# Kernel optimization log

Measured on AMD Instinct MI355X. Metric: run time of the kernel, lower is better.

## Reference

```python
import jax, jax.numpy as jnp
import numpy as np

N_NODES = 50000
N_EDGES = 500000
HIDDEN = 128
HEADS = 8
HEAD_DIM = HIDDEN // HEADS


def setup_inputs() -> dict:
    key = jax.random.key(0)
    ks = jax.random.split(key, 20)

    def lin_w(k, fin, fout):
        return (jax.random.normal(k, (fin, fout), jnp.float32) / np.sqrt(fin)).astype(jnp.float32)

    inp = {
        "h": jax.random.normal(ks[0], (N_NODES, HIDDEN), jnp.float32),
        "x": jax.random.normal(ks[1], (N_NODES, 3), jnp.float32),
        "src": jax.random.randint(ks[2], (N_EDGES,), 0, N_NODES, jnp.int32),
        "dst": jax.random.randint(ks[3], (N_EDGES,), 0, N_NODES, jnp.int32),
        "distances": jax.random.uniform(ks[4], (N_EDGES,), jnp.float32),
        # linear layers stored as [in, out] (transposed vs torch nn.Linear)
        "Wq": lin_w(ks[5], HIDDEN, HIDDEN), "bq": jnp.zeros((HIDDEN,), jnp.float32),
        "Wk": lin_w(ks[6], HIDDEN, HIDDEN), "bk": jnp.zeros((HIDDEN,), jnp.float32),
        "Wv": lin_w(ks[7], HIDDEN, HIDDEN), "bv": jnp.zeros((HIDDEN,), jnp.float32),
        "Wo": lin_w(ks[8], HIDDEN, HIDDEN), "bo": jnp.zeros((HIDDEN,), jnp.float32),
        "Wd": lin_w(ks[9], 1, HEADS), "bd": jnp.zeros((HEADS,), jnp.float32),
        "Wg1": lin_w(ks[10], HIDDEN, HIDDEN), "bg1": jnp.zeros((HIDDEN,), jnp.float32),
        "Wg2": lin_w(ks[11], HIDDEN, 1), "bg2": jnp.zeros((1,), jnp.float32),
    }
    return inp


def reference(h, x, src, dst, distances,
              Wq, bq, Wk, bk, Wv, bv, Wo, bo, Wd, bd, Wg1, bg1, Wg2, bg2):
    n = h.shape[0]
    heads = Wd.shape[1]
    dh = Wq.shape[1] // heads

    q = (h @ Wq + bq).reshape(n, heads, dh)
    k = (h @ Wk + bk).reshape(n, heads, dh)
    v = (h @ Wv + bv).reshape(n, heads, dh)

    q_src = q[src]            # [E, heads, dh]
    k_dst = k[dst]
    v_dst = v[dst]

    logits = jnp.einsum('ehd,ehd->eh', q_src, k_dst) / jnp.sqrt(jnp.asarray(dh, h.dtype))
    bias = (distances * distances)[:, None] @ Wd + bd      # [E, heads]
    lg = logits - bias

    # segment softmax over edges grouped by src node
    m = jax.ops.segment_max(lg, src, num_segments=n)        # [N, heads]
    ex = jnp.exp(lg - m[src])
    s = jax.ops.segment_sum(ex, src, num_segments=n)
    w = ex / jnp.maximum(s[src], 1e-9)                      # [E, heads]

    h_upd = jax.ops.segment_sum(v_dst * w[:, :, None], src, num_segments=n)
    h_out = h + h_upd.reshape(n, heads * dh) @ Wo + bo

    w_mean = w.mean(axis=1)                                 # mean over heads -> [E]
    disp = jax.ops.segment_sum((x[dst] - x[src]) * w_mean[:, None], src, num_segments=n)

    gate = jnp.tanh(jax.nn.silu(h_out @ Wg1 + bg1) @ Wg2 + bg2)  # [N, 1]
    x_out = x + gate * disp
    return (h_out, x_out)
```

## Files before the change

### kernel.cpp

```cpp
#include <hip/hip_runtime.h>
#include <math.h>

#define N_NODES 50000
#define N_EDGES 500000
#define HIDDEN 128
#define HEADS 8
#define HEAD_DIM 16

#define QB 391
#define QKV_TOTAL 782
#define SCAT_BLOCKS 1954
#define SPLITW_BLOCKS 320
#define ZERO_BLOCKS 196

typedef __attribute__((ext_vector_type(8))) short short8;
typedef __attribute__((ext_vector_type(4))) float floatx4;

#define OFF_Q       0u
#define OFF_KV      6400000u
#define OFF_HHI     12800000u
#define OFF_HLO     16000000u
#define OFF_DISP    19200000u
#define OFF_CNT     19350016u
#define OFF_ROWPTR  19400032u
#define OFF_CURSOR  19450048u
#define OFF_ESD     19500064u
#define OFF_WSPLIT  20500064u

static __device__ __forceinline__ unsigned short f2bf(float f) {
    unsigned u = __builtin_bit_cast(unsigned, f);
    unsigned r = (u + 0x7FFFu + ((u >> 16) & 1u)) >> 16;
    return (unsigned short)r;
}
static __device__ __forceinline__ float bf2f(unsigned short s) {
    return __builtin_bit_cast(float, (unsigned)s << 16);
}

__global__ void k_prep(const float* __restrict__ Wq, const float* __restrict__ Wk,
                       const float* __restrict__ Wv, const float* __restrict__ Wo,
                       const float* __restrict__ Wg1, unsigned short* __restrict__ ws,
                       int* __restrict__ cnt) {
    if (blockIdx.x >= SPLITW_BLOCKS) {
        int i = (int)(blockIdx.x - SPLITW_BLOCKS) * 256 + threadIdx.x;
        if (i < N_NODES) cnt[i] = 0;
        return;
    }
    int t = blockIdx.x * 256 + threadIdx.x;
    int m = t >> 14, r = t & 16383;
    int k = r >> 7, n = r & 127;
    const float* W = (m == 0) ? Wq : (m == 1) ? Wk : (m == 2) ? Wv : (m == 3) ? Wo : Wg1;
    float x = W[k * 128 + n];
    int kc = k >> 5, kin = k & 31, quad = kin >> 3, j = kin & 7;
    int ct = n >> 4, nin = n & 15, lane = quad * 16 + nin;
    unsigned base = ((((unsigned)(m * 4 + kc) * 8 + ct) * 2) * 64 + lane) * 8 + j;
    unsigned short a = f2bf(x);
    ws[base] = a;
    ws[base + 512] = f2bf(x - bf2f(a));
}

__global__ void k_count(const int* __restrict__ src, int* __restrict__ cnt,
                        int* __restrict__ rnk) {
    int e = blockIdx.x * 256 + threadIdx.x;
    if (e < N_EDGES) rnk[e] = atomicAdd(&cnt[src[e]], 1);
}

__global__ __launch_bounds__(1024) void k_scan1(const int* __restrict__ cnt,
                                                int* __restrict__ loc,
                                                int* __restrict__ bsum, int n) {
    __shared__ int buf[1024];
    int t = threadIdx.x;
    int i = blockIdx.x * 1024 + t;
    int val = (i < n) ? cnt[i] : 0;
    buf[t] = val;
    __syncthreads();
    for (int off = 1; off < 1024; off <<= 1) {
        int a = (t >= off) ? buf[t - off] : 0;
        __syncthreads();
        buf[t] += a;
        __syncthreads();
    }
    if (i < n) loc[i] = buf[t];
    if (t == 1023) bsum[blockIdx.x] = buf[1023];
}

__global__ __launch_bounds__(256) void k_scan23(const int* __restrict__ loc,
                                                const int* __restrict__ bsum,
                                                int* __restrict__ rowptr, int n, int nb) {
    __shared__ int sb[64];
    int t = threadIdx.x;
    if (t < 64) {
        int v = (t < nb) ? bsum[t] : 0;
        for (int off = 1; off < 64; off <<= 1) {
            int a = __shfl_up(v, off);
            if (t >= off) v += a;
        }
        sb[t] = v;
    }
    __syncthreads();
    int i = blockIdx.x * 256 + t;
    if (i < n) {
        int off = (i >= 1024) ? sb[(i >> 10) - 1] : 0;
        rowptr[i + 1] = loc[i] + off;
    }
    if (i == 0) rowptr[0] = 0;
}

__global__ __launch_bounds__(256, 2) void k_qkv_scatter(
    const float* __restrict__ h, const unsigned short* __restrict__ wsp,
    const float* __restrict__ bq, const float* __restrict__ bk, const float* __restrict__ bv,
    float* __restrict__ q, unsigned* __restrict__ kvp,
    const int* __restrict__ src, const int* __restrict__ dst,
    const float* __restrict__ dist, const int* __restrict__ rowptr,
    const int* __restrict__ rnk, int2* __restrict__ esd) {
    if (blockIdx.x >= QKV_TOTAL) {
        int e = (int)(blockIdx.x - QKV_TOTAL) * 256 + threadIdx.x;
        if (e < N_EDGES) {
            int s = src[e];
            float dd = dist[e];
            int pos = rowptr[s] + rnk[e];
            esd[pos] = make_int2(dst[e], __float_as_int(dd * dd));
        }
        return;
    }

    __shared__ short lds[32768];
    const int tid = threadIdx.x;
    const int wave = tid >> 6, lane = tid & 63;
    const int quad = lane >> 4, l15 = lane & 15;
    const bool iskv = (blockIdx.x >= QB);
    const int blk = iskv ? (int)blockIdx.x - QB : (int)blockIdx.x;
    const int row0 = blk * 128 + wave * 32;

    short8 ah[2][4], al[2][4];
#pragma unroll
    for (int rt = 0; rt < 2; ++rt) {
        int row = row0 + rt * 16 + l15;
        if (row >= N_NODES) row = N_NODES - 1;
        const float* hp = h + (size_t)row * 128;
#pragma unroll
        for (int kc = 0; kc < 4; ++kc) {
            const float* p = hp + kc * 32 + quad * 8;
            float4 f0 = *(const float4*)(p);
            float4 f1 = *(const float4*)(p + 4);
            float fv[8] = {f0.x, f0.y, f0.z, f0.w, f1.x, f1.y, f1.z, f1.w};
#pragma unroll
            for (int j = 0; j < 8; ++j) {
                unsigned short hi = f2bf(fv[j]);
                ah[rt][kc][j] = (short)hi;
                al[rt][kc][j] = (short)f2bf(fv[j] - bf2f(hi));
            }
        }
    }

    auto stage = [&](int m) {
        const float4* s4 = (const float4*)(wsp + (unsigned)m * 32768u);
        float4* d4 = (float4*)lds;
#pragma unroll 4
        for (int it = tid; it < 4096; it += 256) d4[it] = s4[it];
    };

    auto compute = [&](floatx4 (&acc)[2][8]) {
#pragma unroll
        for (int kc = 0; kc < 4; ++kc) {
#pragma unroll
            for (int ct = 0; ct < 8; ++ct) {
                const short* tb = lds + (((kc * 8 + ct) * 2) * 64 + lane) * 8;
                short8 bh = *(const short8*)(tb);
                short8 bl = *(const short8*)(tb + 512);
#pragma unroll
                for (int rt = 0; rt < 2; ++rt) {
                    acc[rt][ct] = __builtin_amdgcn_mfma_f32_16x16x32_bf16(
                        ah[rt][kc], bh, acc[rt][ct], 0, 0, 0);
                    acc[rt][ct] = __builtin_amdgcn_mfma_f32_16x16x32_bf16(
                        ah[rt][kc], bl, acc[rt][ct], 0, 0, 0);
                    acc[rt][ct] = __builtin_amdgcn_mfma_f32_16x16x32_bf16(
                        al[rt][kc], bh, acc[rt][ct], 0, 0, 0);
                }
            }
        }
    };

    if (!iskv) {
        stage(0);
        __syncthreads();
        floatx4 acc[2][8];
#pragma unroll
        for (int rt = 0; rt < 2; ++rt)
#pragma unroll
            for (int ct = 0; ct < 8; ++ct) acc[rt][ct] = (floatx4){0.f, 0.f, 0.f, 0.f};
        compute(acc);
#pragma unroll
        for (int ct = 0; ct < 8; ++ct) {
            int col = ct * 16 + l15;
            float b = bq[col];
#pragma unroll
            for (int rt = 0; rt < 2; ++rt)
#pragma unroll
                for (int reg = 0; reg < 4; ++reg) {
                    int row = row0 + rt * 16 + quad * 4 + reg;
                    if (row < N_NODES) q[(size_t)row * 128 + col] = acc[rt][ct][reg] + b;
                }
        }
    } else {
        stage(1);
        __syncthreads();
        floatx4 acc[2][8];
#pragma unroll
        for (int rt = 0; rt < 2; ++rt)
#pragma unroll
            for (int ct = 0; ct < 8; ++ct) acc[rt][ct] = (floatx4){0.f, 0.f, 0.f, 0.f};
        compute(acc);
        unsigned kb[2][8][2];
#pragma unroll
        for (int ct = 0; ct < 8; ++ct) {
            float b = bk[ct * 16 + l15];
#pragma unroll
            for (int rt = 0; rt < 2; ++rt) {
                kb[rt][ct][0] = (unsigned)f2bf(acc[rt][ct][0] + b) |
                                ((unsigned)f2bf(acc[rt][ct][1] + b) << 16);
                kb[rt][ct][1] = (unsigned)f2bf(acc[rt][ct][2] + b) |
                                ((unsigned)f2bf(acc[rt][ct][3] + b) << 16);
            }
        }
        __syncthreads();
        stage(2);
        __syncthreads();
#pragma unroll
        for (int rt = 0; rt < 2; ++rt)
#pragma unroll
            for (int ct = 0; ct < 8; ++ct) acc[rt][ct] = (floatx4){0.f, 0.f, 0.f, 0.f};
        compute(acc);
#pragma unroll
        for (int ct = 0; ct < 8; ++ct) {
            int col = ct * 16 + l15;
            float b = bv[col];
#pragma unroll
            for (int rt = 0; rt < 2; ++rt)
#pragma unroll
                for (int reg = 0; reg < 4; ++reg) {
                    int row = row0 + rt * 16 + quad * 4 + reg;
                    unsigned vb = f2bf(acc[rt][ct][reg] + b);
                    unsigned kw = (kb[rt][ct][reg >> 1] >> ((reg & 1) * 16)) & 0xFFFFu;
                    if (row < N_NODES) kvp[(size_t)row * 128 + col] = kw | (vb << 16);
                }
        }
    }
}

__global__ __launch_bounds__(256) void k_edge_node(
    const float* __restrict__ q, const unsigned* __restrict__ kvp,
    const float* __restrict__ x,
    const int2* __restrict__ esd, const int* __restrict__ rowptr,
    const float* __restrict__ Wd, const float* __restrict__ bd,
    unsigned short* __restrict__ hupd_hi, unsigned short* __restrict__ hupd_lo,
    float* __restrict__ disp) {
    const int wave = threadIdx.x >> 6, lane = threadIdx.x & 63;
    const int node = blockIdx.x * 4 + wave;
    const int h = lane >> 3, sub = lane & 7;
    const int beg = rowptr[node], end = rowptr[node + 1];

    const float2 qv = *(const float2*)(q + (size_t)node * 128 + 2 * lane);
    const float wdh = Wd[h], bdh = bd[h];
    const bool dal = (sub < 3);
    float xs = dal ? x[node * 3 + sub] : 0.f;
    const unsigned colo = 2 * lane;

    float acc0 = 0.f, acc1 = 0.f, s_own = 0.f, da = 0.f;

    for (int cb = beg; cb < end; cb += 64) {
        int idx = cb + lane;
        int dvec = 0; float d2vec = 0.f;
        if (idx < end) {
            int2 ed = esd[idx];
            dvec = ed.x;
            d2vec = __int_as_float(ed.y);
        }
        int clen = min(64, end - cb);
        int i = 0;
        for (; i + 4 <= clen; i += 4) {
            int di[4]; float dd2[4]; uint2 kv2[4]; float xg[4];
#pragma unroll
            for (int j = 0; j < 4; ++j) {
                di[j]  = __shfl(dvec, i + j);
                dd2[j] = __shfl(d2vec, i + j);
            }
#pragma unroll
            for (int j = 0; j < 4; ++j)
                kv2[j] = *(const uint2*)(kvp + (unsigned)di[j] * 128u + colo);
#pragma unroll
            for (int j = 0; j < 4; ++j)
                xg[j] = dal ? x[(unsigned)di[j] * 3u + sub] : 0.f;
#pragma unroll
            for (int j = 0; j < 4; ++j) {
                float k0 = __builtin_bit_cast(float, kv2[j].x << 16);
                float v0 = __builtin_bit_cast(float, kv2[j].x & 0xFFFF0000u);
                float k1 = __builtin_bit_cast(float, kv2[j].y << 16);
                float v1 = __builtin_bit_cast(float, kv2[j].y & 0xFFFF0000u);
                float p = qv.x * k0 + qv.y * k1;
                p += __shfl_xor(p, 1);
                p += __shfl_xor(p, 2);
                p += __shfl_xor(p, 4);
                float w = __expf(p * 0.25f - (dd2[j] * wdh + bdh));
                s_own += w;
                acc0 += v0 * w;
                acc1 += v1 * w;
                da += (xg[j] - xs) * w;
            }
        }
        for (; i < clen; ++i) {
            int dij  = __shfl(dvec, i);
            float d2 = __shfl(d2vec, i);
            uint2 kv2 = *(const uint2*)(kvp + (unsigned)dij * 128u + colo);
            float xgj = dal ? x[(unsigned)dij * 3u + sub] : 0.f;
            float k0 = __builtin_bit_cast(float, kv2.x << 16);
            float v0 = __builtin_bit_cast(float, kv2.x & 0xFFFF0000u);
            float k1 = __builtin_bit_cast(float, kv2.y << 16);
            float v1 = __builtin_bit_cast(float, kv2.y & 0xFFFF0000u);
            float p = qv.x * k0 + qv.y * k1;
            p += __shfl_xor(p, 1);
            p += __shfl_xor(p, 2);
            p += __shfl_xor(p, 4);
            float w = __expf(p * 0.25f - (d2 * wdh + bdh));
            s_own += w;
            acc0 += v0 * w;
            acc1 += v1 * w;
            da += (xgj - xs) * w;
        }
    }

    float inva = 1.f / fmaxf(s_own, 1e-9f);
    float o0 = acc0 * inva, o1 = acc1 * inva;
    unsigned short h0 = f2bf(o0), h1 = f2bf(o1);
    unsigned short l0 = f2bf(o0 - bf2f(h0)), l1 = f2bf(o1 - bf2f(h1));
    ((unsigned*)hupd_hi)[(size_t)node * 64 + lane] = (unsigned)h0 | ((unsigned)h1 << 16);
    ((unsigned*)hupd_lo)[(size_t)node * 64 + lane] = (unsigned)l0 | ((unsigned)l1 << 16);

    da *= 0.125f * inva;
    da += __shfl_xor(da, 8);
    da += __shfl_xor(da, 16);
    da += __shfl_xor(da, 32);
    if (lane < 3) disp[node * 3 + lane] = da;
}

__global__ __launch_bounds__(256) void k_hout_gate(
    const float* __restrict__ h,
    const unsigned short* __restrict__ hupd_hi, const unsigned short* __restrict__ hupd_lo,
    const unsigned short* __restrict__ wsp,
    const float* __restrict__ bo, const float* __restrict__ bg1,
    const float* __restrict__ Wg2, const float* __restrict__ bg2,
    const float* __restrict__ x, const float* __restrict__ disp,
    float* __restrict__ hout, float* __restrict__ xout) {
    __shared__ float hb[4][16 * 132];
    const int wave = threadIdx.x >> 6, lane = threadIdx.x & 63;
    const int quad = lane >> 4, l15 = lane & 15;
    const int row0 = blockIdx.x * 64 + wave * 16;
    float* hbw = hb[wave];

    floatx4 acc[8];
#pragma unroll
    for (int c = 0; c < 8; ++c) acc[c] = (floatx4){0.f, 0.f, 0.f, 0.f};
#pragma unroll
    for (int kc = 0; kc < 4; ++kc) {
        int row = row0 + l15;
        if (row >= N_NODES) row = N_NODES - 1;
        size_t aoff = (size_t)row * 128 + kc * 32 + quad * 8;
        short8 ah = *(const short8*)(hupd_hi + aoff);
        short8 al = *(const short8*)(hupd_lo + aoff);
#pragma unroll
        for (int ct = 0; ct < 8; ++ct) {
            unsigned fb = ((((unsigned)(3 * 4 + kc) * 8 + ct) * 2) * 64 + lane) * 8;
            short8 bh = *(const short8*)(wsp + fb);
            short8 bl = *(const short8*)(wsp + fb + 512);
            acc[ct] = __builtin_amdgcn_mfma_f32_16x16x32_bf16(ah, bh, acc[ct], 0, 0, 0);
            acc[ct] = __builtin_amdgcn_mfma_f32_16x16x32_bf16(ah, bl, acc[ct], 0, 0, 0);
            acc[ct] = __builtin_amdgcn_mfma_f32_16x16x32_bf16(al, bh, acc[ct], 0, 0, 0);
        }
    }

#pragma unroll
    for (int ct = 0; ct < 8; ++ct) {
        int col = ct * 16 + l15;
        float bias = bo[col];
#pragma unroll
        for (int reg = 0; reg < 4; ++reg) {
            int row = row0 + quad * 4 + reg;
            float val = acc[ct][reg] + bias;
            if (row < N_NODES) {
                val += h[(size_t)row * 128 + col];
                hout[(size_t)row * 128 + col] = val;
            }
            hbw[(quad * 4 + reg) * 132 + col] = val;
        }
    }
    __asm__ volatile("s_waitcnt lgkmcnt(0)" ::: "memory");

    floatx4 acc2[8];
#pragma unroll
    for (int c = 0; c < 8; ++c) acc2[c] = (floatx4){0.f, 0.f, 0.f, 0.f};
#pragma unroll
    for (int kc = 0; kc < 4; ++kc) {
        const float* ap = hbw + l15 * 132 + kc * 32 + quad * 8;
        float4 f0 = *(const float4*)(ap);
        float4 f1 = *(const float4*)(ap + 4);
        float fv[8] = {f0.x, f0.y, f0.z, f0.w, f1.x, f1.y, f1.z, f1.w};
        short8 ah, al;
#pragma unroll
        for (int j = 0; j < 8; ++j) {
            unsigned short hi = f2bf(fv[j]);
            ah[j] = (short)hi;
            al[j] = (short)f2bf(fv[j] - bf2f(hi));
        }
#pragma unroll
        for (int ct = 0; ct < 8; ++ct) {
            unsigned fb = ((((unsigned)(4 * 4 + kc) * 8 + ct) * 2) * 64 + lane) * 8;
            short8 bh = *(const short8*)(wsp + fb);
            short8 bl = *(const short8*)(wsp + fb + 512);
            acc2[ct] = __builtin_amdgcn_mfma_f32_16x16x32_bf16(ah, bh, acc2[ct], 0, 0, 0);
            acc2[ct] = __builtin_amdgcn_mfma_f32_16x16x32_bf16(ah, bl, acc2[ct], 0, 0, 0);
            acc2[ct] = __builtin_amdgcn_mfma_f32_16x16x32_bf16(al, bh, acc2[ct], 0, 0, 0);
        }
    }

    float pr[4] = {0.f, 0.f, 0.f, 0.f};
#pragma unroll
    for (int ct = 0; ct < 8; ++ct) {
        int col = ct * 16 + l15;
        float b1 = bg1[col];
        float w2 = Wg2[col];
#pragma unroll
        for (int reg = 0; reg < 4; ++reg) {
            float z = acc2[ct][reg] + b1;
            pr[reg] += (z / (1.f + __expf(-z))) * w2;
        }
    }
#pragma unroll
    for (int off = 1; off < 16; off <<= 1) {
#pragma unroll
        for (int reg = 0; reg < 4; ++reg) pr[reg] += __shfl_xor(pr[reg], off);
    }
    if (l15 == 0) {
        float b2 = bg2[0];
#pragma unroll
        for (int reg = 0; reg < 4; ++reg) {
            int row = row0 + quad * 4 + reg;
            if (row < N_NODES) {
                float g = tanhf(pr[reg] + b2);
#pragma unroll
                for (int dd = 0; dd < 3; ++dd) {
                    int oo = row * 3 + dd;
                    xout[oo] = x[oo] + g * disp[oo];
                }
            }
        }
    }
}

extern "C" void kernel_launch(void* const* d_in, const int* in_sizes, int n_in,
                              void* d_out, int out_size, void* d_ws, size_t ws_size,
                              hipStream_t stream) {
    const float* h    = (const float*)d_in[0];
    const float* x    = (const float*)d_in[1];
    const int*   src  = (const int*)d_in[2];
    const int*   dst  = (const int*)d_in[3];
    const float* dist = (const float*)d_in[4];
    const float* Wq = (const float*)d_in[5];  const float* bq = (const float*)d_in[6];
    const float* Wk = (const float*)d_in[7];  const float* bk = (const float*)d_in[8];
    const float* Wv = (const float*)d_in[9];  const float* bv = (const float*)d_in[10];
    const float* Wo = (const float*)d_in[11]; const float* bo = (const float*)d_in[12];
    const float* Wd = (const float*)d_in[13]; const float* bd = (const float*)d_in[14];
    const float* Wg1 = (const float*)d_in[15]; const float* bg1 = (const float*)d_in[16];
    const float* Wg2 = (const float*)d_in[17]; const float* bg2 = (const float*)d_in[18];

    float* ws    = (float*)d_ws;
    float* q     = ws + OFF_Q;
    unsigned* kvp = (unsigned*)(ws + OFF_KV);
    float* disp  = ws + OFF_DISP;
    int* cnt     = (int*)(ws + OFF_CNT);
    int* rowptr  = (int*)(ws + OFF_ROWPTR);
    int2* esd    = (int2*)(ws + OFF_ESD);
    unsigned short* wsp = (unsigned short*)(ws + OFF_WSPLIT);
    int* loc    = (int*)(ws + OFF_Q);
    int* bsum   = (int*)(ws + OFF_Q + 500000u);
    int* rank   = (int*)(ws + OFF_HHI);
    unsigned short* hupd_hi = (unsigned short*)(ws + OFF_HHI);
    unsigned short* hupd_lo = (unsigned short*)(ws + OFF_HLO);
    float* hout = (float*)d_out;
    float* xout = hout + (size_t)N_NODES * HIDDEN;

    const int nscan = (N_NODES + 1023) / 1024;

    k_prep<<<SPLITW_BLOCKS + ZERO_BLOCKS, 256, 0, stream>>>(Wq, Wk, Wv, Wo, Wg1, wsp, cnt);
    k_count<<<SCAT_BLOCKS, 256, 0, stream>>>(src, cnt, rank);
    k_scan1<<<nscan, 1024, 0, stream>>>(cnt, loc, bsum, N_NODES);
    k_scan23<<<ZERO_BLOCKS, 256, 0, stream>>>(loc, bsum, rowptr, N_NODES, nscan);
    k_qkv_scatter<<<QKV_TOTAL + SCAT_BLOCKS, 256, 0, stream>>>(
        h, wsp, bq, bk, bv, q, kvp, src, dst, dist, rowptr, rank, esd);
    k_edge_node<<<N_NODES / 4, 256, 0, stream>>>(q, kvp, x, esd, rowptr,
                                                 Wd, bd, hupd_hi, hupd_lo, disp);
    k_hout_gate<<<(N_NODES + 63) / 64, 256, 0, stream>>>(h, hupd_hi, hupd_lo, wsp,
                                                         bo, bg1, Wg2, bg2,
                                                         x, disp, hout, xout);
}
```

Measured before the change: 259.8 us.

## Use persistent atomic work queue for edge kernel and halve QKV LDS staging

The edge/node aggregation kernel becomes persistent: a fixed grid of waves pulls node indices from a global atomic cursor, reset in the scan kernel, instead of launching one wave per node. Edge records are now read directly per edge rather than loaded cooperatively and broadcast by shuffle. The 1/sqrt(dh) scale is folded into q once, and bd is dropped from the exponent, which is only valid because it cancels in the softmax. The QKV GEMM stages weights in two half-K chunks so LDS per block is halved and occupancy can rise to 4 blocks per CU, at the cost of extra barriers and one atomic per node.

After: 893.1 us. 244% more time.

```diff
diff --git a/kernel.cpp b/kernel.cpp
--- a/kernel.cpp
+++ b/kernel.cpp
@@ -12,6 +12,7 @@
 #define SCAT_BLOCKS 1954
 #define SPLITW_BLOCKS 320
 #define ZERO_BLOCKS 196
+#define EN_BLOCKS 1563
 
 typedef __attribute__((ext_vector_type(8))) short short8;
 typedef __attribute__((ext_vector_type(4))) float floatx4;
@@ -85,7 +86,8 @@
 
 __global__ __launch_bounds__(256) void k_scan23(const int* __restrict__ loc,
                                                 const int* __restrict__ bsum,
-                                                int* __restrict__ rowptr, int n, int nb) {
+                                                int* __restrict__ rowptr,
+                                                int* __restrict__ cursor, int n, int nb) {
     __shared__ int sb[64];
     int t = threadIdx.x;
     if (t < 64) {
@@ -102,10 +104,10 @@
         int off = (i >= 1024) ? sb[(i >> 10) - 1] : 0;
         rowptr[i + 1] = loc[i] + off;
     }
-    if (i == 0) rowptr[0] = 0;
-}
-
-__global__ __launch_bounds__(256, 2) void k_qkv_scatter(
+    if (i == 0) { rowptr[0] = 0; cursor[0] = 0; }
+}
+
+__global__ __launch_bounds__(256, 4) void k_qkv_scatter(
     const float* __restrict__ h, const unsigned short* __restrict__ wsp,
     const float* __restrict__ bq, const float* __restrict__ bk, const float* __restrict__ bv,
     float* __restrict__ q, unsigned* __restrict__ kvp,
@@ -123,7 +125,7 @@
         return;
     }
 
-    __shared__ short lds[32768];
+    __shared__ short lds[16384];
     const int tid = threadIdx.x;
     const int wave = tid >> 6, lane = tid & 63;
     const int quad = lane >> 4, l15 = lane & 15;
@@ -152,19 +154,20 @@
         }
     }
 
-    auto stage = [&](int m) {
-        const float4* s4 = (const float4*)(wsp + (unsigned)m * 32768u);
+    auto stageh = [&](int m, int hh) {
+        const float4* s4 = (const float4*)(wsp + (unsigned)m * 32768u + (unsigned)hh * 16384u);
         float4* d4 = (float4*)lds;
 #pragma unroll 4
-        for (int it = tid; it < 4096; it += 256) d4[it] = s4[it];
+        for (int it = tid; it < 2048; it += 256) d4[it] = s4[it];
     };
 
-    auto compute = [&](floatx4 (&acc)[2][8]) {
-#pragma unroll
-        for (int kc = 0; kc < 4; ++kc) {
+    auto computeh = [&](floatx4 (&acc)[2][8], int hh) {
+#pragma unroll
+        for (int kcl = 0; kcl < 2; ++kcl) {
+            const int kc = hh * 2 + kcl;
 #pragma unroll
             for (int ct = 0; ct < 8; ++ct) {
-                const short* tb = lds + (((kc * 8 + ct) * 2) * 64 + lane) * 8;
+                const short* tb = lds + (((kcl * 8 + ct) * 2) * 64 + lane) * 8;
                 short8 bh = *(const short8*)(tb);
                 short8 bl = *(const short8*)(tb + 512);
 #pragma unroll
@@ -181,14 +184,15 @@
     };
 
     if (!iskv) {
-        stage(0);
-        __syncthreads();
         floatx4 acc[2][8];
 #pragma unroll
         for (int rt = 0; rt < 2; ++rt)
 #pragma unroll
             for (int ct = 0; ct < 8; ++ct) acc[rt][ct] = (floatx4){0.f, 0.f, 0.f, 0.f};
-        compute(acc);
+        stageh(0, 0); __syncthreads();
+        computeh(acc, 0); __syncthreads();
+        stageh(0, 1); __syncthreads();
+        computeh(acc, 1);
 #pragma unroll
         for (int ct = 0; ct < 8; ++ct) {
             int col = ct * 16 + l15;
@@ -202,14 +206,15 @@
                 }
         }
     } else {
-        stage(1);
-        __syncthreads();
         floatx4 acc[2][8];
 #pragma unroll
         for (int rt = 0; rt < 2; ++rt)
 #pragma unroll
             for (int ct = 0; ct < 8; ++ct) acc[rt][ct] = (floatx4){0.f, 0.f, 0.f, 0.f};
-        compute(acc);
+        stageh(1, 0); __syncthreads();
+        computeh(acc, 0); __syncthreads();
+        stageh(1, 1); __syncthreads();
+        computeh(acc, 1);
         unsigned kb[2][8][2];
 #pragma unroll
         for (int ct = 0; ct < 8; ++ct) {
@@ -223,13 +228,14 @@
             }
         }
         __syncthreads();
-        stage(2);
-        __syncthreads();
 #pragma unroll
         for (int rt = 0; rt < 2; ++rt)
 #pragma unroll
             for (int ct = 0; ct < 8; ++ct) acc[rt][ct] = (floatx4){0.f, 0.f, 0.f, 0.f};
-        compute(acc);
+        stageh(2, 0); __syncthreads();
+        computeh(acc, 0); __syncthreads();
+        stageh(2, 1); __syncthreads();
+        computeh(acc, 1);
 #pragma unroll
         for (int ct = 0; ct < 8; ++ct) {
             int col = ct * 16 + l15;
@@ -252,44 +258,39 @@
     const float* __restrict__ x,
     const int2* __restrict__ esd, const int* __restrict__ rowptr,
     const float* __restrict__ Wd, const float* __restrict__ bd,
+    int* __restrict__ cursor,
     unsigned short* __restrict__ hupd_hi, unsigned short* __restrict__ hupd_lo,
     float* __restrict__ disp) {
-    const int wave = threadIdx.x >> 6, lane = threadIdx.x & 63;
-    const int node = blockIdx.x * 4 + wave;
+    const int lane = threadIdx.x & 63;
     const int h = lane >> 3, sub = lane & 7;
-    const int beg = rowptr[node], end = rowptr[node + 1];
-
-    const float2 qv = *(const float2*)(q + (size_t)node * 128 + 2 * lane);
-    const float wdh = Wd[h], bdh = bd[h];
+    const float wdh = Wd[h];
     const bool dal = (sub < 3);
-    float xs = dal ? x[node * 3 + sub] : 0.f;
     const unsigned colo = 2 * lane;
 
-    float acc0 = 0.f, acc1 = 0.f, s_own = 0.f, da = 0.f;
-
-    for (int cb = beg; cb < end; cb += 64) {
-        int idx = cb + lane;
-        int dvec = 0; float d2vec = 0.f;
-        if (idx < end) {
-            int2 ed = esd[idx];
-            dvec = ed.x;
-            d2vec = __int_as_float(ed.y);
-        }
-        int clen = min(64, end - cb);
-        int i = 0;
-        for (; i + 4 <= clen; i += 4) {
-            int di[4]; float dd2[4]; uint2 kv2[4]; float xg[4];
-#pragma unroll
-            for (int j = 0; j < 4; ++j) {
-                di[j]  = __shfl(dvec, i + j);
-                dd2[j] = __shfl(d2vec, i + j);
-            }
+    while (true) {
+        int node = 0;
+        if (lane == 0) node = atomicAdd(cursor, 1);
+        node = __shfl(node, 0);
+        if (node >= N_NODES) break;
+
+        const int beg = rowptr[node], end = rowptr[node + 1];
+        float2 qv = *(const float2*)(q + (size_t)node * 128 + 2 * lane);
+        qv.x *= 0.25f; qv.y *= 0.25f;
+        float xs = dal ? x[node * 3 + sub] : 0.f;
+
+        float acc0 = 0.f, acc1 = 0.f, s_own = 0.f, da = 0.f;
+
+        int e = beg;
+        for (; e + 4 <= end; e += 4) {
+            int2 ed[4]; uint2 kv2[4]; float xg[4];
+#pragma unroll
+            for (int j = 0; j < 4; ++j) ed[j] = esd[e + j];
 #pragma unroll
             for (int j = 0; j < 4; ++j)
-                kv2[j] = *(const uint2*)(kvp + (unsigned)di[j] * 128u + colo);
+                kv2[j] = *(const uint2*)(kvp + (unsigned)ed[j].x * 128u + colo);
 #pragma unroll
             for (int j = 0; j < 4; ++j)
-                xg[j] = dal ? x[(unsigned)di[j] * 3u + sub] : 0.f;
+                xg[j] = dal ? x[(unsigned)ed[j].x * 3u + sub] : 0.f;
 #pragma unroll
             for (int j = 0; j < 4; ++j) {
                 float k0 = __builtin_bit_cast(float, kv2[j].x << 16);
@@ -300,18 +301,17 @@
                 p += __shfl_xor(p, 1);
                 p += __shfl_xor(p, 2);
                 p += __shfl_xor(p, 4);
-                float w = __expf(p * 0.25f - (dd2[j] * wdh + bdh));
+                float w = __expf(p - __int_as_float(ed[j].y) * wdh);
                 s_own += w;
                 acc0 += v0 * w;
                 acc1 += v1 * w;
                 da += (xg[j] - xs) * w;
             }
         }
-        for (; i < clen; ++i) {
-            int dij  = __shfl(dvec, i);
-            float d2 = __shfl(d2vec, i);
-            uint2 kv2 = *(const uint2*)(kvp + (unsigned)dij * 128u + colo);
-            float xgj = dal ? x[(unsigned)dij * 3u + sub] : 0.f;
+        for (; e < end; ++e) {
+            int2 ed = esd[e];
+            uint2 kv2 = *(const uint2*)(kvp + (unsigned)ed.x * 128u + colo);
+            float xgj = dal ? x[(unsigned)ed.x * 3u + sub] : 0.f;
             float k0 = __builtin_bit_cast(float, kv2.x << 16);
             float v0 = __builtin_bit_cast(float, kv2.x & 0xFFFF0000u);
             float k1 = __builtin_bit_cast(float, kv2.y << 16);
@@ -320,26 +320,26 @@
             p += __shfl_xor(p, 1);
             p += __shfl_xor(p, 2);
             p += __shfl_xor(p, 4);
-            float w = __expf(p * 0.25f - (d2 * wdh + bdh));
+            float w = __expf(p - __int_as_float(ed.y) * wdh);
             s_own += w;
             acc0 += v0 * w;
             acc1 += v1 * w;
             da += (xgj - xs) * w;
         }
-    }
-
-    float inva = 1.f / fmaxf(s_own, 1e-9f);
-    float o0 = acc0 * inva, o1 = acc1 * inva;
-    unsigned short h0 = f2bf(o0), h1 = f2bf(o1);
-    unsigned short l0 = f2bf(o0 - bf2f(h0)), l1 = f2bf(o1 - bf2f(h1));
-    ((unsigned*)hupd_hi)[(size_t)node * 64 + lane] = (unsigned)h0 | ((unsigned)h1 << 16);
-    ((unsigned*)hupd_lo)[(size_t)node * 64 + lane] = (unsigned)l0 | ((unsigned)l1 << 16);
-
-    da *= 0.125f * inva;
-    da += __shfl_xor(da, 8);
-    da += __shfl_xor(da, 16);
-    da += __shfl_xor(da, 32);
-    if (lane < 3) disp[node * 3 + lane] = da;
+
+        float inva = 1.f / fmaxf(s_own, 1e-9f);
+        float o0 = acc0 * inva, o1 = acc1 * inva;
+        unsigned short h0 = f2bf(o0), h1 = f2bf(o1);
+        unsigned short l0 = f2bf(o0 - bf2f(h0)), l1 = f2bf(o1 - bf2f(h1));
+        ((unsigned*)hupd_hi)[(size_t)node * 64 + lane] = (unsigned)h0 | ((unsigned)h1 << 16);
+        ((unsigned*)hupd_lo)[(size_t)node * 64 + lane] = (unsigned)l0 | ((unsigned)l1 << 16);
+
+        da *= 0.125f * inva;
+        da += __shfl_xor(da, 8);
+        da += __shfl_xor(da, 16);
+        da += __shfl_xor(da, 32);
+        if (lane < 3) disp[node * 3 + lane] = da;
+    }
 }
 
 __global__ __launch_bounds__(256) void k_hout_gate(
@@ -477,6 +477,7 @@
     float* disp  = ws + OFF_DISP;
     int* cnt     = (int*)(ws + OFF_CNT);
     int* rowptr  = (int*)(ws + OFF_ROWPTR);
+    int* cursor  = (int*)(ws + OFF_CURSOR);
     int2* esd    = (int2*)(ws + OFF_ESD);
     unsigned short* wsp = (unsigned short*)(ws + OFF_WSPLIT);
     int* loc    = (int*)(ws + OFF_Q);
@@ -492,11 +493,11 @@
     k_prep<<<SPLITW_BLOCKS + ZERO_BLOCKS, 256, 0, stream>>>(Wq, Wk, Wv, Wo, Wg1, wsp, cnt);
     k_count<<<SCAT_BLOCKS, 256, 0, stream>>>(src, cnt, rank);
     k_scan1<<<nscan, 1024, 0, stream>>>(cnt, loc, bsum, N_NODES);
-    k_scan23<<<ZERO_BLOCKS, 256, 0, stream>>>(loc, bsum, rowptr, N_NODES, nscan);
+    k_scan23<<<ZERO_BLOCKS, 256, 0, stream>>>(loc, bsum, rowptr, cursor, N_NODES, nscan);
     k_qkv_scatter<<<QKV_TOTAL + SCAT_BLOCKS, 256, 0, stream>>>(
         h, wsp, bq, bk, bv, q, kvp, src, dst, dist, rowptr, rank, esd);
-    k_edge_node<<<N_NODES / 4, 256, 0, stream>>>(q, kvp, x, esd, rowptr,
-                                                 Wd, bd, hupd_hi, hupd_lo, disp);
+    k_edge_node<<<EN_BLOCKS, 256, 0, stream>>>(q, kvp, x, esd, rowptr,
+                                               Wd, bd, cursor, hupd_hi, hupd_lo, disp);
     k_hout_gate<<<(N_NODES + 63) / 64, 256, 0, stream>>>(h, hupd_hi, hupd_lo, wsp,
                                                          bo, bg1, Wg2, bg2,
                                                          x, disp, hout, xout);
```
